# Kernel tuning notes

Measured on AMD Instinct MI355X. Metric: run time of the kernel, lower is better.

Reference implementation:

```python
import jax, jax.numpy as jnp
import numpy as np

B = 16384  # batch size
DN = ('NCHW', 'OIHW', 'NCHW')


def maxpool2(x):
    # 2x2 max pool, stride 2, VALID (matches nn.MaxPool2d(2, 2))
    return jax.lax.reduce_window(x, -jnp.inf, jax.lax.max,
                                 (1, 1, 2, 2), (1, 1, 2, 2), 'VALID')


def setup_inputs() -> dict:
    key = jax.random.key(0)
    ks = jax.random.split(key, 7)
    return {
        'x': jax.random.normal(ks[0], (B, 1, 32, 32), jnp.float32),
        'w1': jax.random.normal(ks[1], (6, 1, 5, 5), jnp.float32) * 0.1,
        'w2': jax.random.normal(ks[2], (16, 6, 5, 5), jnp.float32) * 0.1,
        'fw1': jax.random.normal(ks[3], (120, 400), jnp.float32) * 0.05,
        'fw2': jax.random.normal(ks[4], (84, 120), jnp.float32) * 0.05,
        'fc3_w': jax.random.normal(ks[5], (10, 84), jnp.float32) * 0.1,
        'fc3_b': jax.random.normal(ks[6], (10,), jnp.float32) * 0.1,
    }


def reference(x, w1, w2, fw1, fw2, fc3_w, fc3_b):
    # conv1 (no bias in StdConv2D) -> relu -> pool
    h = jax.lax.conv_general_dilated(x, w1, (1, 1), 'VALID', dimension_numbers=DN)
    h = maxpool2(jax.nn.relu(h))                      # [B,6,14,14]
    # conv2 -> relu -> pool
    h = jax.lax.conv_general_dilated(h, w2, (1, 1), 'VALID', dimension_numbers=DN)
    h = maxpool2(jax.nn.relu(h))                      # [B,16,5,5]
    h = h.reshape(h.shape[0], 400)                    # channel-major flatten, as torch view
    # StdFC layers: x @ W.T, no bias
    h = jax.nn.relu(h @ fw1.T)                        # [B,120]
    h = jax.nn.relu(h @ fw2.T)                        # [B,84]
    logits = h @ fc3_w.T + fc3_b                      # nn.Linear fc3 with bias
    return jax.nn.softmax(logits, axis=1)
```

## Files before the change

kernel.cpp:

```cpp
#include <hip/hip_runtime.h>
#include <math.h>

#define TH 256

typedef __attribute__((ext_vector_type(8))) short short8;
typedef __attribute__((ext_vector_type(4))) float floatx4;

#define P1_S   0
#define XBUF_F 4704
#define P2_S   9408
#define H1_S   12800
#define H2_S   13888
#define LOG_F  7360
#define W1_F   7968
#define BT_S   16240
#define LDS_F  9464

static __device__ __forceinline__ unsigned short f2bf(float x) {
    union { float f; unsigned u; } v; v.f = x;
    unsigned r = (v.u + 0x7FFFu + ((v.u >> 16) & 1u)) >> 16;
    return (unsigned short)r;
}

static __device__ __forceinline__ short8 load_bf8_clamped(const float* row, int kb, int K) {
    int b0 = (kb + 4 <= K) ? kb : (K - 8);
    int b1 = (kb + 8 <= K) ? (kb + 4) : (K - 8);
    float4 w0 = *(const float4*)(row + b0);
    float4 w1 = *(const float4*)(row + b1);
    short8 b;
    b[0] = (short)f2bf(w0.x); b[1] = (short)f2bf(w0.y);
    b[2] = (short)f2bf(w0.z); b[3] = (short)f2bf(w0.w);
    b[4] = (short)f2bf(w1.x); b[5] = (short)f2bf(w1.y);
    b[6] = (short)f2bf(w1.z); b[7] = (short)f2bf(w1.w);
    return b;
}

__global__ __launch_bounds__(TH) void lenet_kernel(
    const float* __restrict__ x,
    const float* __restrict__ w1,
    const float* __restrict__ w2g,
    const float* __restrict__ fw1,
    const float* __restrict__ fw2,
    const float* __restrict__ fc3w,
    const float* __restrict__ fc3b,
    float* __restrict__ out)
{
    __shared__ __align__(16) float sf[LDS_F];
    short* sh = (short*)sf;
    const int* p1i = (const int*)sf;

    const int tid  = threadIdx.x;
    const int blk  = blockIdx.x;
    const int lane = tid & 63;
    const int wid  = tid >> 6;
    const int g    = lane >> 4;
    const int cn   = lane & 15;

    for (int sub = 0; sub < 3; ++sub) {
        const int nimg = (sub < 2) ? 3 : 2;
        const float* xg = x + ((size_t)blk * 8 + sub * 3) * 1024;
        for (int e = tid; e < nimg * 256; e += TH) {
            int m = e >> 8, rem = e & 255;
            int y = rem >> 3, k4 = rem & 7;
            float4 v = ((const float4*)xg)[e];
            int d = XBUF_F + m * 1088 + y * 34 + k4 * 4;
            *(float2*)(sf + d)     = make_float2(v.x, v.y);
            *(float2*)(sf + d + 2) = make_float2(v.z, v.w);
        }
        if (sub == 0) {
            for (int e = tid; e < 150; e += TH) sf[W1_F + e] = w1[e];
            for (int e = tid; e < 2560; e += TH) {
                int oc = e / 160, kk = e - oc * 160;
                int s = kk >> 5, r = kk & 31;
                float v = 0.f;
                if (r < 30) v = w2g[oc * 150 + (r % 6) * 25 + s * 5 + (r / 6)];
                sh[BT_S + oc * 168 + kk] = (short)f2bf(v);
            }
        }
        __syncthreads();

        const int ntask = nimg * 168;
        for (int t = tid; t < ntask; t += TH) {
            int m = t / 168, r = t - m * 168;
            int c = r % 6, q = r / 6;
            int i = q >> 1, hf = q & 1;
            const float* xm = sf + XBUF_F + m * 1088 + hf * 14;
            const float* wc = sf + W1_F + c * 25;
            float acc0[14], acc1[14];
            #pragma unroll
            for (int j = 0; j < 14; ++j) { acc0[j] = 0.f; acc1[j] = 0.f; }
            #pragma unroll
            for (int tt = 0; tt < 6; ++tt) {
                float row[18];
                const float* rp = xm + (2 * i + tt) * 34;
                #pragma unroll
                for (int qq = 0; qq < 9; ++qq) {
                    float2 v2 = *(const float2*)(rp + 2 * qq);
                    row[2 * qq] = v2.x; row[2 * qq + 1] = v2.y;
                }
                if (tt < 5) {
                    #pragma unroll
                    for (int kx = 0; kx < 5; ++kx) {
                        float w = wc[tt * 5 + kx];
                        #pragma unroll
                        for (int xx = 0; xx < 14; ++xx)
                            acc0[xx] = fmaf(row[xx + kx], w, acc0[xx]);
                    }
                }
                if (tt >= 1) {
                    #pragma unroll
                    for (int kx = 0; kx < 5; ++kx) {
                        float w = wc[(tt - 1) * 5 + kx];
                        #pragma unroll
                        for (int xx = 0; xx < 14; ++xx)
                            acc1[xx] = fmaf(row[xx + kx], w, acc1[xx]);
                    }
                }
            }
            int gi = sub * 3 + m;
            #pragma unroll
            for (int j = 0; j < 7; ++j) {
                float v = fmaxf(fmaxf(acc0[2 * j], acc0[2 * j + 1]),
                                fmaxf(acc1[2 * j], acc1[2 * j + 1]));
                v = fmaxf(v, 0.f);
                sh[P1_S + gi * 1176 + i * 84 + (7 * hf + j) * 6 + c] = (short)f2bf(v);
            }
        }
        __syncthreads();
    }

    {
        short8 Breg[5];
        #pragma unroll
        for (int s = 0; s < 5; ++s)
            Breg[s] = *(const short8*)(sh + BT_S + cn * 168 + s * 32 + 8 * g);

        for (int e = tid; e < 8 * 24; e += TH) {
            int im = e / 24;
            sh[P2_S + im * 424 + 400 + (e - im * 24)] = 0;
        }

        for (int w = wid; w < 25; w += 4) {
            int i = w / 5, jx = w - 5 * i;
            floatx4 a00 = {0.f,0.f,0.f,0.f}, a01 = {0.f,0.f,0.f,0.f};
            floatx4 a10 = {0.f,0.f,0.f,0.f}, a11 = {0.f,0.f,0.f,0.f};
            #pragma unroll
            for (int s = 0; s < 5; ++s) {
                #pragma unroll
                for (int dy = 0; dy < 2; ++dy) {
                    #pragma unroll
                    for (int dx = 0; dx < 2; ++dx) {
                        int as = cn * 1176 + (2 * i + dy + s) * 84 + (2 * jx + dx) * 6 + 8 * g;
                        int ai = as >> 1;
                        short8 a;
                        int* av = (int*)&a;
                        av[0] = p1i[ai]; av[1] = p1i[ai + 1];
                        av[2] = p1i[ai + 2]; av[3] = p1i[ai + 3];
                        floatx4* acc = dy == 0 ? (dx == 0 ? &a00 : &a01)
                                               : (dx == 0 ? &a10 : &a11);
                        *acc = __builtin_amdgcn_mfma_f32_16x16x32_bf16(a, Breg[s], *acc, 0, 0, 0);
                    }
                }
            }
            if (g < 2) {
                #pragma unroll
                for (int rg = 0; rg < 4; ++rg) {
                    float v = fmaxf(fmaxf(a00[rg], a01[rg]), fmaxf(a10[rg], a11[rg]));
                    v = fmaxf(v, 0.f);
                    int im = 4 * g + rg;
                    sh[P2_S + im * 424 + cn * 25 + i * 5 + jx] = (short)f2bf(v);
                }
            }
        }
    }
    __syncthreads();

    {
        for (int e = tid; e < 8 * 16; e += TH) {
            int im = e >> 4;
            sh[H1_S + im * 136 + 120 + (e & 15)] = 0;
        }
        for (int nt = wid; nt < 8; nt += 4) {
            floatx4 acc = {0.f,0.f,0.f,0.f};
            int n = nt * 16 + cn;
            const float* wrow = fw1 + (size_t)(n < 120 ? n : 119) * 400;
            for (int ks = 0; ks < 13; ++ks) {
                int kb = ks * 32 + 8 * g;
                short8 b = load_bf8_clamped(wrow, kb, 400);
                short8 a = *(const short8*)(sh + P2_S + cn * 424 + kb);
                acc = __builtin_amdgcn_mfma_f32_16x16x32_bf16(a, b, acc, 0, 0, 0);
            }
            if (g < 2 && n < 120) {
                #pragma unroll
                for (int rg = 0; rg < 4; ++rg)
                    sh[H1_S + (4 * g + rg) * 136 + n] = (short)f2bf(fmaxf(acc[rg], 0.f));
            }
        }
    }
    __syncthreads();

    {
        for (int e = tid; e < 8 * 20; e += TH) {
            int im = e / 20;
            sh[H2_S + im * 104 + 84 + (e - im * 20)] = 0;
        }
        for (int nt = wid; nt < 6; nt += 4) {
            floatx4 acc = {0.f,0.f,0.f,0.f};
            int n = nt * 16 + cn;
            const float* wrow = fw2 + (size_t)(n < 84 ? n : 83) * 120;
            for (int ks = 0; ks < 4; ++ks) {
                int kb = ks * 32 + 8 * g;
                short8 b = load_bf8_clamped(wrow, kb, 120);
                short8 a = *(const short8*)(sh + H1_S + cn * 136 + kb);
                acc = __builtin_amdgcn_mfma_f32_16x16x32_bf16(a, b, acc, 0, 0, 0);
            }
            if (g < 2 && n < 84) {
                #pragma unroll
                for (int rg = 0; rg < 4; ++rg)
                    sh[H2_S + (4 * g + rg) * 104 + n] = (short)f2bf(fmaxf(acc[rg], 0.f));
            }
        }
    }
    __syncthreads();

    if (wid == 0) {
        floatx4 acc = {0.f,0.f,0.f,0.f};
        int n = cn;
        const float* wrow = fc3w + (size_t)(n < 10 ? n : 9) * 84;
        for (int ks = 0; ks < 3; ++ks) {
            int kb = ks * 32 + 8 * g;
            short8 b = load_bf8_clamped(wrow, kb, 84);
            short8 a = *(const short8*)(sh + H2_S + cn * 104 + kb);
            acc = __builtin_amdgcn_mfma_f32_16x16x32_bf16(a, b, acc, 0, 0, 0);
        }
        if (g < 2 && n < 10) {
            float bias = fc3b[n];
            #pragma unroll
            for (int rg = 0; rg < 4; ++rg)
                sf[LOG_F + (4 * g + rg) * 12 + n] = acc[rg] + bias;
        }
    }
    __syncthreads();

    if (tid < 8) {
        const float* lg = sf + LOG_F + tid * 12;
        float mx = lg[0];
        #pragma unroll
        for (int n = 1; n < 10; ++n) mx = fmaxf(mx, lg[n]);
        float e[10]; float sum = 0.f;
        #pragma unroll
        for (int n = 0; n < 10; ++n) { e[n] = expf(lg[n] - mx); sum += e[n]; }
        float inv = 1.f / sum;
        float* op = out + ((size_t)blk * 8 + tid) * 10;
        #pragma unroll
        for (int n = 0; n < 10; ++n) op[n] = e[n] * inv;
    }
}

extern "C" void kernel_launch(void* const* d_in, const int* in_sizes, int n_in,
                              void* d_out, int out_size, void* d_ws, size_t ws_size,
                              hipStream_t stream) {
    const float* x    = (const float*)d_in[0];
    const float* w1   = (const float*)d_in[1];
    const float* w2   = (const float*)d_in[2];
    const float* fw1  = (const float*)d_in[3];
    const float* fw2  = (const float*)d_in[4];
    const float* fc3w = (const float*)d_in[5];
    const float* fc3b = (const float*)d_in[6];
    float* outp = (float*)d_out;

    dim3 grid(16384 / 8), block(TH);
    hipLaunchKernelGGL(lenet_kernel, grid, block, 0, stream,
                       x, w1, w2, fw1, fw2, fc3w, fc3b, outp);
}
```

Measured before the change: 102.7 us.

## Compute conv1 in packed fp16, shrink LDS, truncate weight conversion to bf16

Stores input images and conv1 weights as fp16 in LDS and computes conv1 with packed half2 FMAs (two output columns per instruction, shifted pairs built with byte perms). This halves conv1 FMA count and LDS footprint. The LDS layout is reorganised with aliasing regions and a padded P1 stride, and MFMA A rows now use cn&7 so rows 8-15 read duplicate valid data instead of uninitialised rows. Weight float-to-bf16 conversion for the FC layers switches to truncation via perm, which is cheaper but less accurate. fp16 accumulation over 25 taps also risks precision loss.

```diff
diff --git a/kernel.cpp b/kernel.cpp
--- a/kernel.cpp
+++ b/kernel.cpp
@@ -1,4 +1,5 @@
 #include <hip/hip_runtime.h>
+#include <hip/hip_fp16.h>
 #include <math.h>
 
 #define TH 256
@@ -7,32 +8,36 @@
 typedef __attribute__((ext_vector_type(4))) float floatx4;
 
 #define P1_S   0
-#define XBUF_F 4704
-#define P2_S   9408
-#define H1_S   12800
-#define H2_S   13888
-#define LOG_F  7360
-#define W1_F   7968
-#define BT_S   16240
-#define LDS_F  9464
+#define X_S    9424
+#define P2_S   9424
+#define BT_S   12816
+#define H1_S   12816
+#define H2_S   13904
+#define LOG_F  7368
+#define W1B_U  7752
+#define LDS_F  7904
 
 static __device__ __forceinline__ unsigned short f2bf(float x) {
     union { float f; unsigned u; } v; v.f = x;
-    unsigned r = (v.u + 0x7FFFu + ((v.u >> 16) & 1u)) >> 16;
-    return (unsigned short)r;
-}
-
-static __device__ __forceinline__ short8 load_bf8_clamped(const float* row, int kb, int K) {
+    return (unsigned short)((v.u + 0x7FFFu + ((v.u >> 16) & 1u)) >> 16);
+}
+static __device__ __forceinline__ __half2 uash2(unsigned u) {
+    union { unsigned u; __half2 h; } v; v.u = u; return v.h;
+}
+static __device__ __forceinline__ unsigned bfpack(unsigned hi, unsigned lo) {
+    return __builtin_amdgcn_perm(hi, lo, 0x07060302u);
+}
+static __device__ __forceinline__ short8 load_bf8t(const float* row, int kb, int K) {
     int b0 = (kb + 4 <= K) ? kb : (K - 8);
     int b1 = (kb + 8 <= K) ? (kb + 4) : (K - 8);
-    float4 w0 = *(const float4*)(row + b0);
-    float4 w1 = *(const float4*)(row + b1);
-    short8 b;
-    b[0] = (short)f2bf(w0.x); b[1] = (short)f2bf(w0.y);
-    b[2] = (short)f2bf(w0.z); b[3] = (short)f2bf(w0.w);
-    b[4] = (short)f2bf(w1.x); b[5] = (short)f2bf(w1.y);
-    b[6] = (short)f2bf(w1.z); b[7] = (short)f2bf(w1.w);
-    return b;
+    uint4 w0 = *(const uint4*)(row + b0);
+    uint4 w1 = *(const uint4*)(row + b1);
+    union { int4 i; short8 s; } r;
+    r.i.x = (int)bfpack(w0.y, w0.x);
+    r.i.y = (int)bfpack(w0.w, w0.z);
+    r.i.z = (int)bfpack(w1.y, w1.x);
+    r.i.w = (int)bfpack(w1.w, w1.z);
+    return r.s;
 }
 
 __global__ __launch_bounds__(TH) void lenet_kernel(
@@ -47,6 +52,7 @@
 {
     __shared__ __align__(16) float sf[LDS_F];
     short* sh = (short*)sf;
+    unsigned* su = (unsigned*)sf;
     const int* p1i = (const int*)sf;
 
     const int tid  = threadIdx.x;
@@ -55,20 +61,22 @@
     const int wid  = tid >> 6;
     const int g    = lane >> 4;
     const int cn   = lane & 15;
+    const int pr   = cn & 7;
 
     for (int sub = 0; sub < 3; ++sub) {
         const int nimg = (sub < 2) ? 3 : 2;
-        const float* xg = x + ((size_t)blk * 8 + sub * 3) * 1024;
+        const float4* xg = (const float4*)(x + ((size_t)blk * 8 + sub * 3) * 1024);
         for (int e = tid; e < nimg * 256; e += TH) {
-            int m = e >> 8, rem = e & 255;
-            int y = rem >> 3, k4 = rem & 7;
-            float4 v = ((const float4*)xg)[e];
-            int d = XBUF_F + m * 1088 + y * 34 + k4 * 4;
-            *(float2*)(sf + d)     = make_float2(v.x, v.y);
-            *(float2*)(sf + d + 2) = make_float2(v.z, v.w);
+            float4 v = xg[e];
+            int off = X_S + e * 4;
+            *(__half2*)(sh + off)     = __floats2half2_rn(v.x, v.y);
+            *(__half2*)(sh + off + 2) = __floats2half2_rn(v.z, v.w);
         }
         if (sub == 0) {
-            for (int e = tid; e < 150; e += TH) sf[W1_F + e] = w1[e];
+            for (int e = tid; e < 150; e += TH) {
+                __half h = __float2half(w1[e]);
+                ((__half2*)(su + W1B_U))[e] = __half2half2(h);
+            }
             for (int e = tid; e < 2560; e += TH) {
                 int oc = e / 160, kk = e - oc * 160;
                 int s = kk >> 5, r = kk & 31;
@@ -84,46 +92,71 @@
             int m = t / 168, r = t - m * 168;
             int c = r % 6, q = r / 6;
             int i = q >> 1, hf = q & 1;
-            const float* xm = sf + XBUF_F + m * 1088 + hf * 14;
-            const float* wc = sf + W1_F + c * 25;
-            float acc0[14], acc1[14];
-            #pragma unroll
-            for (int j = 0; j < 14; ++j) { acc0[j] = 0.f; acc1[j] = 0.f; }
+            const __half2* wb = (const __half2*)(su + W1B_U) + c * 25;
+            const int xbase = X_S + m * 1024 + hf * 14;
+
+            __half2 acc0[7], acc1[7];
+            #pragma unroll
+            for (int j = 0; j < 7; ++j) { acc0[j] = uash2(0u); acc1[j] = uash2(0u); }
+            __half2 wprev[5];
             #pragma unroll
             for (int tt = 0; tt < 6; ++tt) {
-                float row[18];
-                const float* rp = xm + (2 * i + tt) * 34;
-                #pragma unroll
-                for (int qq = 0; qq < 9; ++qq) {
-                    float2 v2 = *(const float2*)(rp + 2 * qq);
-                    row[2 * qq] = v2.x; row[2 * qq + 1] = v2.y;
-                }
+                unsigned u[9];
+                const unsigned* rp = (const unsigned*)(sh + xbase + (2 * i + tt) * 32);
+                #pragma unroll
+                for (int qq = 0; qq < 9; ++qq) u[qq] = rp[qq];
+                __half2 p0[9], p1[8];
+                #pragma unroll
+                for (int qq = 0; qq < 9; ++qq) p0[qq] = uash2(u[qq]);
+                #pragma unroll
+                for (int qq = 0; qq < 8; ++qq)
+                    p1[qq] = uash2(__builtin_amdgcn_perm(u[qq + 1], u[qq], 0x05040302u));
+
                 if (tt < 5) {
-                    #pragma unroll
-                    for (int kx = 0; kx < 5; ++kx) {
-                        float w = wc[tt * 5 + kx];
+                    __half2 wc[5];
+                    #pragma unroll
+                    for (int kx = 0; kx < 5; ++kx) wc[kx] = wb[tt * 5 + kx];
+                    #pragma unroll
+                    for (int j = 0; j < 7; ++j) {
+                        acc0[j] = __hfma2(p0[j],     wc[0], acc0[j]);
+                        acc0[j] = __hfma2(p1[j],     wc[1], acc0[j]);
+                        acc0[j] = __hfma2(p0[j + 1], wc[2], acc0[j]);
+                        acc0[j] = __hfma2(p1[j + 1], wc[3], acc0[j]);
+                        acc0[j] = __hfma2(p0[j + 2], wc[4], acc0[j]);
+                    }
+                    if (tt >= 1) {
                         #pragma unroll
-                        for (int xx = 0; xx < 14; ++xx)
-                            acc0[xx] = fmaf(row[xx + kx], w, acc0[xx]);
+                        for (int j = 0; j < 7; ++j) {
+                            acc1[j] = __hfma2(p0[j],     wprev[0], acc1[j]);
+                            acc1[j] = __hfma2(p1[j],     wprev[1], acc1[j]);
+                            acc1[j] = __hfma2(p0[j + 1], wprev[2], acc1[j]);
+                            acc1[j] = __hfma2(p1[j + 1], wprev[3], acc1[j]);
+                            acc1[j] = __hfma2(p0[j + 2], wprev[4], acc1[j]);
+                        }
+                    }
+                    #pragma unroll
+                    for (int kx = 0; kx < 5; ++kx) wprev[kx] = wc[kx];
+                } else {
+                    #pragma unroll
+                    for (int j = 0; j < 7; ++j) {
+                        acc1[j] = __hfma2(p0[j],     wprev[0], acc1[j]);
+                        acc1[j] = __hfma2(p1[j],     wprev[1], acc1[j]);
+                        acc1[j] = __hfma2(p0[j + 1], wprev[2], acc1[j]);
+                        acc1[j] = __hfma2(p1[j + 1], wprev[3], acc1[j]);
+                        acc1[j] = __hfma2(p0[j + 2], wprev[4], acc1[j]);
                     }
                 }
-                if (tt >= 1) {
-                    #pragma unroll
-                    for (int kx = 0; kx < 5; ++kx) {
-                        float w = wc[(tt - 1) * 5 + kx];
-                        #pragma unroll
-                        for (int xx = 0; xx < 14; ++xx)
-                            acc1[xx] = fmaf(row[xx + kx], w, acc1[xx]);
-                    }
-                }
             }
             int gi = sub * 3 + m;
+            short* dst = sh + P1_S + gi * 1178 + i * 84 + hf * 42 + c;
             #pragma unroll
             for (int j = 0; j < 7; ++j) {
-                float v = fmaxf(fmaxf(acc0[2 * j], acc0[2 * j + 1]),
-                                fmaxf(acc1[2 * j], acc1[2 * j + 1]));
-                v = fmaxf(v, 0.f);
-                sh[P1_S + gi * 1176 + i * 84 + (7 * hf + j) * 6 + c] = (short)f2bf(v);
+                float a0l = __half2float(__low2half(acc0[j]));
+                float a0h = __half2float(__high2half(acc0[j]));
+                float a1l = __half2float(__low2half(acc1[j]));
+                float a1h = __half2float(__high2half(acc1[j]));
+                float v = fmaxf(fmaxf(fmaxf(a0l, a0h), fmaxf(a1l, a1h)), 0.f);
+                dst[j * 6] = (short)f2bf(v);
             }
         }
         __syncthreads();
@@ -150,15 +183,14 @@
                 for (int dy = 0; dy < 2; ++dy) {
                     #pragma unroll
                     for (int dx = 0; dx < 2; ++dx) {
-                        int as = cn * 1176 + (2 * i + dy + s) * 84 + (2 * jx + dx) * 6 + 8 * g;
+                        int as = pr * 1178 + (2 * i + dy + s) * 84 + (2 * jx + dx) * 6 + 8 * g;
                         int ai = as >> 1;
-                        short8 a;
-                        int* av = (int*)&a;
-                        av[0] = p1i[ai]; av[1] = p1i[ai + 1];
-                        av[2] = p1i[ai + 2]; av[3] = p1i[ai + 3];
+                        union { int4 i4; short8 s8; } a;
+                        a.i4.x = p1i[ai];     a.i4.y = p1i[ai + 1];
+                        a.i4.z = p1i[ai + 2]; a.i4.w = p1i[ai + 3];
                         floatx4* acc = dy == 0 ? (dx == 0 ? &a00 : &a01)
                                                : (dx == 0 ? &a10 : &a11);
-                        *acc = __builtin_amdgcn_mfma_f32_16x16x32_bf16(a, Breg[s], *acc, 0, 0, 0);
+                        *acc = __builtin_amdgcn_mfma_f32_16x16x32_bf16(a.s8, Breg[s], *acc, 0, 0, 0);
                     }
                 }
             }
@@ -186,8 +218,8 @@
             const float* wrow = fw1 + (size_t)(n < 120 ? n : 119) * 400;
             for (int ks = 0; ks < 13; ++ks) {
                 int kb = ks * 32 + 8 * g;
-                short8 b = load_bf8_clamped(wrow, kb, 400);
-                short8 a = *(const short8*)(sh + P2_S + cn * 424 + kb);
+                short8 b = load_bf8t(wrow, kb, 400);
+                short8 a = *(const short8*)(sh + P2_S + pr * 424 + kb);
                 acc = __builtin_amdgcn_mfma_f32_16x16x32_bf16(a, b, acc, 0, 0, 0);
             }
             if (g < 2 && n < 120) {
@@ -210,8 +242,8 @@
             const float* wrow = fw2 + (size_t)(n < 84 ? n : 83) * 120;
             for (int ks = 0; ks < 4; ++ks) {
                 int kb = ks * 32 + 8 * g;
-                short8 b = load_bf8_clamped(wrow, kb, 120);
-                short8 a = *(const short8*)(sh + H1_S + cn * 136 + kb);
+                short8 b = load_bf8t(wrow, kb, 120);
+                short8 a = *(const short8*)(sh + H1_S + pr * 136 + kb);
                 acc = __builtin_amdgcn_mfma_f32_16x16x32_bf16(a, b, acc, 0, 0, 0);
             }
             if (g < 2 && n < 84) {
@@ -229,8 +261,8 @@
         const float* wrow = fc3w + (size_t)(n < 10 ? n : 9) * 84;
         for (int ks = 0; ks < 3; ++ks) {
             int kb = ks * 32 + 8 * g;
-            short8 b = load_bf8_clamped(wrow, kb, 84);
-            short8 a = *(const short8*)(sh + H2_S + cn * 104 + kb);
+            short8 b = load_bf8t(wrow, kb, 84);
+            short8 a = *(const short8*)(sh + H2_S + pr * 104 + kb);
             acc = __builtin_amdgcn_mfma_f32_16x16x32_bf16(a, b, acc, 0, 0, 0);
         }
         if (g < 2 && n < 10) {
```

Measured after the change: 88.21 us. 1.16x faster.
